# Optimization experiments

Hardware: AMD Instinct MI355X
Metric: run time of the kernel (lower is better)

The kernel has to match this reference:

```python
import jax, jax.numpy as jnp
import numpy as np

T_MAX = 0.5
LN_EPS = 1e-5
B, N, D = 256, 16384, 512
NNZ = N * 33  # ~ (2*top_k+1) nonzeros per row of the sparse Laplacian
DF = 4 * D
DT = 32  # time-embedding hidden size


def _layernorm(x, g, b):
    mu = jnp.mean(x, axis=-1, keepdims=True)
    var = jnp.mean((x - mu) ** 2, axis=-1, keepdims=True)
    return (x - mu) * jax.lax.rsqrt(var + LN_EPS) * g + b


def setup_inputs() -> dict:
    key = jax.random.key(0)
    ks = jax.random.split(key, 16)

    def lin_w(k, fan_out, fan_in):
        return jax.random.normal(k, (fan_out, fan_in), jnp.float32) * (1.0 / np.sqrt(fan_in))

    inp = {}
    inp["x0"] = jax.random.uniform(ks[0], (B, N), jnp.float32)
    inp["t"] = jax.random.uniform(ks[1], (B,), jnp.float32)
    inp["L_vals"] = jax.random.normal(ks[2], (NNZ,), jnp.float32) * 0.1
    inp["W_in"] = lin_w(ks[3], D, N)
    inp["b_in"] = jnp.zeros((D,), jnp.float32)
    inp["W_out"] = lin_w(ks[4], N, D)
    inp["b_out"] = jnp.zeros((N,), jnp.float32)
    inp["W_qkv"] = lin_w(ks[5], 3 * D, D)
    inp["b_qkv"] = jnp.zeros((3 * D,), jnp.float32)
    inp["W_o"] = lin_w(ks[6], D, D)
    inp["b_o"] = jnp.zeros((D,), jnp.float32)
    inp["g1"] = jnp.ones((D,), jnp.float32)
    inp["be1"] = jnp.zeros((D,), jnp.float32)
    inp["g2"] = jnp.ones((D,), jnp.float32)
    inp["be2"] = jnp.zeros((D,), jnp.float32)
    inp["W_f1"] = lin_w(ks[7], DF, D)
    inp["b_f1"] = jnp.zeros((DF,), jnp.float32)
    inp["W_f2"] = lin_w(ks[8], D, DF)
    inp["b_f2"] = jnp.zeros((D,), jnp.float32)
    inp["W_t1"] = lin_w(ks[9], DT, 1)
    inp["b_t1"] = jnp.zeros((DT,), jnp.float32)
    inp["W_t2"] = lin_w(ks[10], D, DT)
    inp["b_t2"] = jnp.zeros((D,), jnp.float32)
    inp["L_rows"] = jax.random.randint(ks[11], (NNZ,), 0, N, jnp.int32)
    inp["L_cols"] = jax.random.randint(ks[12], (NNZ,), 0, N, jnp.int32)
    return inp


def reference(x0, t, L_vals, W_in, b_in, W_out, b_out, W_qkv, b_qkv, W_o, b_o,
              g1, be1, g2, be2, W_f1, b_f1, W_f2, b_f2, W_t1, b_t1, W_t2, b_t2,
              L_rows, L_cols):
    n_items = x0.shape[1]
    d_model = W_in.shape[0]
    t_cont = t * T_MAX  # per-sample diffusion time (explicit input, not RNG)

    # Batched sparse Laplacian diffusion (replaces the per-row torch.sparse.mm loop):
    # (L @ x.T)[i, b] = sum_e L_vals[e] * x0[b, L_cols[e]] aggregated to row L_rows[e]
    contrib = x0[:, L_cols] * L_vals                                  # (B, NNZ)
    Lx = jax.ops.segment_sum(contrib.T, L_rows, num_segments=n_items)  # (N, B)
    x_t = x0 - t_cont[:, None] * Lx.T                                  # (B, N)

    # Denoiser (eval mode: dropout off)
    h = x_t @ W_in.T + b_in                                            # (B, D)
    t_norm = t_cont / T_MAX
    te = jax.nn.silu(t_norm[:, None] @ W_t1.T + b_t1) @ W_t2.T + b_t2  # (B, D)
    h = h + te

    # MultiheadAttention on a length-1 sequence: softmax over one key is exactly 1,
    # so attn_out = out_proj(V) with V = h @ W_v.T + b_v.
    qkv = h @ W_qkv.T + b_qkv                                          # (B, 3D)
    v = qkv[:, 2 * d_model:]
    attn_out = v @ W_o.T + b_o

    h = _layernorm(h + attn_out, g1, be1)
    ff = jax.nn.gelu(h @ W_f1.T + b_f1, approximate=False) @ W_f2.T + b_f2
    h = _layernorm(h + ff, g2, be2)

    pred = h @ W_out.T + b_out                                         # (B, N)
    return jnp.mean((pred - x0) ** 2)
```

## Files before the change

### kernel.cpp

```cpp
#include <hip/hip_runtime.h>
#include <math.h>

#define Bb   256
#define Nn   16384
#define Dd   512
#define NNZn 540672
#define DFf  2048
#define SLOT 64

#define CVT_BLKS 4736
#define TR_BLKS  1024
#define BK_BLKS  2112
#define PREP_BLKS (CVT_BLKS + TR_BLKS + BK_BLKS)

#define C1 65536
#define C2 131072
#define C3 393216
#define C4 655360
#define C5 2752512
#define C6 4849664

typedef __bf16 bf16;
typedef __bf16 bf16x4 __attribute__((ext_vector_type(4)));
typedef __bf16 bf16x8 __attribute__((ext_vector_type(8)));
typedef float  f32x4  __attribute__((ext_vector_type(4)));

__device__ __forceinline__ void gload16(const void* g, void* l) {
  __builtin_amdgcn_global_load_lds(
      (const __attribute__((address_space(1))) unsigned int*)g,
      (__attribute__((address_space(3))) unsigned int*)l, 16, 0, 0);
}

template <int NK>
__device__ __forceinline__ void bar_keep() {
  asm volatile("s_waitcnt vmcnt(%0) lgkmcnt(0)" :: "n"(NK) : "memory");
  __builtin_amdgcn_s_barrier();
}

__device__ __forceinline__ float f16_of(unsigned e) {
  unsigned short us = (unsigned short)(e & 0xffff);
  _Float16 h;
  __builtin_memcpy(&h, &us, 2);
  return (float)h;
}

__global__ __launch_bounds__(256) void k_prep(
    const float* __restrict__ w_v, const float* __restrict__ w_o,
    const float* __restrict__ w_f1, const float* __restrict__ w_f2,
    const float* __restrict__ w_in, const float* __restrict__ w_out,
    bf16* __restrict__ o_v, bf16* __restrict__ o_o,
    bf16* __restrict__ o_f1, bf16* __restrict__ o_f2,
    bf16* __restrict__ o_in, bf16* __restrict__ o_out,
    const float* __restrict__ x0, bf16* __restrict__ x0T,
    const int* __restrict__ rows, const int* __restrict__ cols,
    const float* __restrict__ vals,
    int* __restrict__ counts, unsigned* __restrict__ ents) {
  __shared__ float tile[64][65];
  int blk = blockIdx.x;
  int q = blk / 3;
  if ((blk % 3) == 0 && q < BK_BLKS) {
    int i = q * 256 + threadIdx.x;
    int r = rows[i];
    int p = atomicAdd(&counts[r], 1);
    if (p < SLOT) {
      _Float16 hv = (_Float16)vals[i];
      unsigned short us;
      __builtin_memcpy(&us, &hv, 2);
      ents[(size_t)r * SLOT + p] = ((unsigned)cols[i] << 16) | (unsigned)us;
    }
  } else {
    int sB = (blk + 2) / 3; if (sB > BK_BLKS) sB = BK_BLKS;
    int o = blk - sB;
    if (o < CVT_BLKS) {
      int v0i = o * 1024 + threadIdx.x;
#pragma unroll
      for (int j = 0; j < 4; j++) {
        int v = v0i + j * 256;
        const float* s; bf16* d; int base;
        if (v < C2)      { if (v < C1) { s = w_v;  d = o_v;  base = 0;  }
                           else        { s = w_o;  d = o_o;  base = C1; } }
        else if (v < C4) { if (v < C3) { s = w_f1; d = o_f1; base = C2; }
                           else        { s = w_f2; d = o_f2; base = C3; } }
        else             { if (v < C5) { s = w_in; d = o_in; base = C4; }
                           else        { s = w_out; d = o_out; base = C5; } }
        int idx = (v - base) * 4;
        float4 x = *(const float4*)(s + idx);
        bf16x4 ob;
        ob[0] = (bf16)x.x; ob[1] = (bf16)x.y; ob[2] = (bf16)x.z; ob[3] = (bf16)x.w;
        *(bf16x4*)(d + idx) = ob;
      }
    } else {
      int bx = o - CVT_BLKS;
      int n0 = (bx & 255) * 64, b0 = (bx >> 8) * 64;
      int tx = threadIdx.x & 63, ty = threadIdx.x >> 6;
#pragma unroll
      for (int i = 0; i < 16; i++) {
        int bl = ty * 16 + i;
        tile[bl][tx] = x0[(size_t)(b0 + bl) * Nn + n0 + tx];
      }
      __syncthreads();
#pragma unroll
      for (int i = 0; i < 16; i++) {
        int nl = ty * 16 + i;
        x0T[(size_t)(n0 + nl) * Bb + b0 + tx] = (bf16)tile[tx][nl];
      }
    }
  }
}

__global__ __launch_bounds__(256) void k_lx(const bf16x4* __restrict__ x0T4,
                                            const int* __restrict__ counts,
                                            const unsigned* __restrict__ ents,
                                            bf16x4* __restrict__ Lx4) {
  int w = threadIdx.x >> 6, lane = threadIdx.x & 63;
  int r = blockIdx.x * 4 + w;
  __shared__ unsigned esm[4][64];
  int cnt = counts[r];
  if (cnt > SLOT) cnt = SLOT;
  const unsigned* ep = ents + (size_t)r * SLOT;
  float a0 = 0.f, a1 = 0.f, a2 = 0.f, a3 = 0.f;
  float b0 = 0.f, b1 = 0.f, b2 = 0.f, b3 = 0.f;
  float c0 = 0.f, c1 = 0.f, c2 = 0.f, c3 = 0.f;
  float d0 = 0.f, d1 = 0.f, d2 = 0.f, d3 = 0.f;
  for (int base = 0; base < cnt; base += 64) {
    int m = cnt - base; if (m > 64) m = 64;
    if (lane < m) esm[w][lane] = ep[base + lane];
    int i = 0;
    for (; i + 3 < m; i += 4) {
      unsigned e0 = esm[w][i],     e1 = esm[w][i + 1];
      unsigned e2 = esm[w][i + 2], e3 = esm[w][i + 3];
      bf16x4 xv0 = x0T4[(size_t)(e0 >> 16) * 64 + lane];
      bf16x4 xv1 = x0T4[(size_t)(e1 >> 16) * 64 + lane];
      bf16x4 xv2 = x0T4[(size_t)(e2 >> 16) * 64 + lane];
      bf16x4 xv3 = x0T4[(size_t)(e3 >> 16) * 64 + lane];
      float v0 = f16_of(e0), v1 = f16_of(e1), v2 = f16_of(e2), v3 = f16_of(e3);
      a0 += v0 * (float)xv0[0]; a1 += v0 * (float)xv0[1];
      a2 += v0 * (float)xv0[2]; a3 += v0 * (float)xv0[3];
      b0 += v1 * (float)xv1[0]; b1 += v1 * (float)xv1[1];
      b2 += v1 * (float)xv1[2]; b3 += v1 * (float)xv1[3];
      c0 += v2 * (float)xv2[0]; c1 += v2 * (float)xv2[1];
      c2 += v2 * (float)xv2[2]; c3 += v2 * (float)xv2[3];
      d0 += v3 * (float)xv3[0]; d1 += v3 * (float)xv3[1];
      d2 += v3 * (float)xv3[2]; d3 += v3 * (float)xv3[3];
    }
    for (; i < m; i++) {
      unsigned e0 = esm[w][i];
      bf16x4 xv0 = x0T4[(size_t)(e0 >> 16) * 64 + lane];
      float v0 = f16_of(e0);
      a0 += v0 * (float)xv0[0]; a1 += v0 * (float)xv0[1];
      a2 += v0 * (float)xv0[2]; a3 += v0 * (float)xv0[3];
    }
  }
  bf16x4 o;
  o[0] = (bf16)(a0 + b0 + c0 + d0); o[1] = (bf16)(a1 + b1 + c1 + d1);
  o[2] = (bf16)(a2 + b2 + c2 + d2); o[3] = (bf16)(a3 + b3 + c3 + d3);
  Lx4[(size_t)r * 64 + lane] = o;
}

__global__ __launch_bounds__(256) void k_combine(const float* __restrict__ x0,
                                                 const bf16* __restrict__ Lx,
                                                 const float* __restrict__ t,
                                                 bf16* __restrict__ xt) {
  __shared__ float lxs[64][65];
  int n0 = blockIdx.x * 64, b0 = blockIdx.y * 64;
  int tx = threadIdx.x & 63, ty = threadIdx.x >> 6;
#pragma unroll
  for (int i = 0; i < 16; i++) {
    int nl = ty * 16 + i;
    lxs[nl][tx] = (float)Lx[(size_t)(n0 + nl) * Bb + b0 + tx];
  }
  __syncthreads();
#pragma unroll
  for (int i = 0; i < 16; i++) {
    int bl = ty * 16 + i;
    int b  = b0 + bl;
    float tc = t[b] * 0.5f;
    float v = x0[(size_t)b * Nn + n0 + tx] - tc * lxs[tx][bl];
    xt[(size_t)b * Nn + n0 + tx] = (bf16)v;
  }
}

template <int BM, int BN, int MODE, int ACT = 0>
__global__ __launch_bounds__(256) void gemm_tn(
    const bf16* __restrict__ A, const bf16* __restrict__ Bm,
    float* __restrict__ C, int N, int K, int kLen, int MN,
    const float* __restrict__ bias, const float* __restrict__ x0,
    float* __restrict__ lossOut) {
  constexpr int WM = BM / 2, WN = BN / 2, FM = WM / 16, FN = WN / 16;
  constexpr int PASS = (BM + BN) / 64;
  constexpr int KEEP = PASS;
  __shared__ __align__(16) bf16 As[3][BM * 32];
  __shared__ __align__(16) bf16 Bs[3][BN * 32];
  __shared__ float lred[4];
  const int tid = threadIdx.x;
  const int lane = tid & 63, w = tid >> 6;
  const int wm = w >> 1, wn = w & 1;
  const int mBase = blockIdx.x * BM, nBase = blockIdx.y * BN;
  const int k0 = blockIdx.z * kLen;
  const int nIter = kLen >> 5;

  f32x4 acc[FM][FN];
#pragma unroll
  for (int i = 0; i < FM; i++)
#pragma unroll
    for (int j = 0; j < FN; j++) acc[i][j] = {0.f, 0.f, 0.f, 0.f};

  auto stage = [&](int buf, int k) {
#pragma unroll
    for (int p = 0; p < PASS; p++) {
      int c = p * 4 + w;
      int u = c * 64 + lane;
      if (c < BM / 16) {
        int row = u >> 2, sub = u & 3;
        gload16(A + (size_t)(mBase + row) * K + k + sub * 8,
                (char*)As[buf] + c * 1024);
      } else {
        int u2 = u - BM * 4;
        int row = u2 >> 2, sub = u2 & 3;
        gload16(Bm + (size_t)(nBase + row) * K + k + sub * 8,
                (char*)Bs[buf] + (c - BM / 16) * 1024);
      }
    }
  };
  auto compute = [&](int cur) {
    bf16x8 af[FM], bfr[FN];
#pragma unroll
    for (int i = 0; i < FM; i++)
      af[i] = *(const bf16x8*)(As[cur] + (wm * WM + i * 16 + (lane & 15)) * 32 + (lane >> 4) * 8);
#pragma unroll
    for (int j = 0; j < FN; j++)
      bfr[j] = *(const bf16x8*)(Bs[cur] + (wn * WN + j * 16 + (lane & 15)) * 32 + (lane >> 4) * 8);
#pragma unroll
    for (int i = 0; i < FM; i++)
#pragma unroll
      for (int j = 0; j < FN; j++)
        acc[i][j] = __builtin_amdgcn_mfma_f32_16x16x32_bf16(af[i], bfr[j], acc[i][j], 0, 0, 0);
  };

  stage(0, k0);
  if (nIter > 1) {
    stage(1, k0 + 32);
    bar_keep<KEEP>();
  } else {
    bar_keep<0>();
  }

  int c0 = 0, c1 = 1, c2 = 2;
  for (int t = 0; t < nIter; t += 2) {
    {
      const bool more2 = (t + 2 < nIter);
      if (more2) stage(c2, k0 + (t + 2) * 32);
      compute(c0);
      if (more2) bar_keep<KEEP>(); else bar_keep<0>();
    }
    {
      const bool more2 = (t + 3 < nIter);
      if (more2) stage(c0, k0 + (t + 3) * 32);
      compute(c1);
      if (more2) bar_keep<KEEP>(); else bar_keep<0>();
    }
    int tmp = c2; c2 = c1; c1 = c0; c0 = tmp;
  }

  if constexpr (MODE == 0) {
    float* Cz = C + (size_t)blockIdx.z * MN;
#pragma unroll
    for (int i = 0; i < FM; i++)
#pragma unroll
      for (int j = 0; j < FN; j++) {
        int n  = nBase + wn * WN + j * 16 + (lane & 15);
        int mB = mBase + wm * WM + i * 16 + ((lane >> 4) << 2);
#pragma unroll
        for (int r = 0; r < 4; r++)
          Cz[(size_t)(mB + r) * N + n] = acc[i][j][r];
      }
  } else if constexpr (MODE == 1) {
    bf16* Cb = (bf16*)C;
#pragma unroll
    for (int i = 0; i < FM; i++)
#pragma unroll
      for (int j = 0; j < FN; j++) {
        int n  = nBase + wn * WN + j * 16 + (lane & 15);
        float bo = bias[n];
        int mB = mBase + wm * WM + i * 16 + ((lane >> 4) << 2);
#pragma unroll
        for (int r = 0; r < 4; r++) {
          float x = acc[i][j][r] + bo;
          if constexpr (ACT == 1)
            x = 0.5f * x * (1.f + erff(x * 0.70710678118654752f));
          Cb[(size_t)(mB + r) * N + n] = (bf16)x;
        }
      }
  } else {
    float lsum = 0.f;
#pragma unroll
    for (int i = 0; i < FM; i++)
#pragma unroll
      for (int j = 0; j < FN; j++) {
        int n  = nBase + wn * WN + j * 16 + (lane & 15);
        float bo = bias[n];
        int mB = mBase + wm * WM + i * 16 + ((lane >> 4) << 2);
#pragma unroll
        for (int r = 0; r < 4; r++) {
          float d = acc[i][j][r] + bo - x0[(size_t)(mB + r) * N + n];
          lsum += d * d;
        }
      }
    for (int off = 32; off > 0; off >>= 1) lsum += __shfl_down(lsum, off, 64);
    if (lane == 0) lred[w] = lsum;
    __syncthreads();
    if (tid == 0)
      atomicAdd(lossOut, lred[0] + lred[1] + lred[2] + lred[3]);
  }
}

__global__ __launch_bounds__(512) void k_epi_h(const float* __restrict__ P,
                                               const float* __restrict__ t,
                                               const float* __restrict__ W_t1,
                                               const float* __restrict__ b_t1,
                                               const float* __restrict__ W_t2,
                                               const float* __restrict__ b_t2,
                                               const float* __restrict__ b_in,
                                               float* __restrict__ h_f32,
                                               bf16* __restrict__ h_b) {
  int b = blockIdx.x, d = threadIdx.x;
  __shared__ float s[32];
  if (d < 32) {
    float z = t[b] * W_t1[d] + b_t1[d];
    s[d] = z / (1.f + expf(-z));
  }
  __syncthreads();
  int i = b * Dd + d;
  float v = b_in[d] + b_t2[d];
#pragma unroll
  for (int sp = 0; sp < 32; sp++) v += P[sp * (Bb * Dd) + i];
#pragma unroll
  for (int j = 0; j < 32; j++) v += s[j] * W_t2[d * 32 + j];
  h_f32[i] = v;
  h_b[i] = (bf16)v;
}

template <int NS>
__global__ __launch_bounds__(512) void k_ln(const float* __restrict__ base,
                                            const float* __restrict__ add,
                                            const float* __restrict__ bias,
                                            const float* __restrict__ g,
                                            const float* __restrict__ be,
                                            float* __restrict__ out_f32,
                                            bf16* __restrict__ out_b) {
  int b = blockIdx.x, d = threadIdx.x;
  __shared__ float red[16];
  int i = b * Dd + d;
  float x = base[i] + bias[d];
#pragma unroll
  for (int sp = 0; sp < NS; sp++) x += add[sp * (Bb * Dd) + i];
  int w = d >> 6, lane = d & 63;
  float s = x;
  for (int off = 32; off > 0; off >>= 1) s += __shfl_down(s, off, 64);
  if (lane == 0) red[w] = s;
  __syncthreads();
  if (d == 0) {
    float tot = 0.f;
    for (int q = 0; q < 8; q++) tot += red[q];
    red[8] = tot * (1.f / 512.f);
  }
  __syncthreads();
  float mu = red[8];
  float c = x - mu;
  float s2 = c * c;
  for (int off = 32; off > 0; off >>= 1) s2 += __shfl_down(s2, off, 64);
  if (lane == 0) red[w] = s2;
  __syncthreads();
  if (d == 0) {
    float tot = 0.f;
    for (int q = 0; q < 8; q++) tot += red[q];
    red[8] = tot * (1.f / 512.f);
  }
  __syncthreads();
  float var = red[8];
  float y = c * rsqrtf(var + 1e-5f) * g[d] + be[d];
  if (out_f32) out_f32[i] = y;
  out_b[i] = (bf16)y;
}

__global__ void k_final(const float* __restrict__ loss, float* __restrict__ out) {
  if (threadIdx.x == 0 && blockIdx.x == 0)
    out[0] = loss[0] * (1.f / 4194304.f);
}

extern "C" void kernel_launch(void* const* d_in, const int* in_sizes, int n_in,
                              void* d_out, int out_size, void* d_ws, size_t ws_size,
                              hipStream_t stream) {
  const float* x0    = (const float*)d_in[0];
  const float* t     = (const float*)d_in[1];
  const float* Lv    = (const float*)d_in[2];
  const float* W_in  = (const float*)d_in[3];
  const float* b_in  = (const float*)d_in[4];
  const float* W_out = (const float*)d_in[5];
  const float* b_out = (const float*)d_in[6];
  const float* W_qkv = (const float*)d_in[7];
  const float* b_qkv = (const float*)d_in[8];
  const float* W_o   = (const float*)d_in[9];
  const float* b_o   = (const float*)d_in[10];
  const float* g1    = (const float*)d_in[11];
  const float* be1   = (const float*)d_in[12];
  const float* g2    = (const float*)d_in[13];
  const float* be2   = (const float*)d_in[14];
  const float* W_f1  = (const float*)d_in[15];
  const float* b_f1  = (const float*)d_in[16];
  const float* W_f2  = (const float*)d_in[17];
  const float* b_f2  = (const float*)d_in[18];
  const float* W_t1  = (const float*)d_in[19];
  const float* b_t1  = (const float*)d_in[20];
  const float* W_t2  = (const float*)d_in[21];
  const float* b_t2  = (const float*)d_in[22];
  const int* L_rows  = (const int*)d_in[23];
  const int* L_cols  = (const int*)d_in[24];

  size_t off = 0;
  char* ws = (char*)d_ws;
  auto carve = [&](size_t bytes) -> void* {
    void* p = ws + off;
    off += (bytes + 255) & ~(size_t)255;
    return p;
  };

  bf16* W_v_b    = (bf16*)carve((size_t)Dd * Dd * 2);
  bf16* W_o_b    = (bf16*)carve((size_t)Dd * Dd * 2);
  bf16* W_f1_b   = (bf16*)carve((size_t)DFf * Dd * 2);
  bf16* W_f2_b   = (bf16*)carve((size_t)Dd * DFf * 2);
  bf16* W_in_b   = (bf16*)carve((size_t)Dd * Nn * 2);
  bf16* W_out_b  = (bf16*)carve((size_t)Nn * Dd * 2);
  bf16* x0T_b    = (bf16*)carve((size_t)Nn * Bb * 2);
  bf16* Lx_b     = (bf16*)carve((size_t)Nn * Bb * 2);
  bf16* xt_b     = (bf16*)carve((size_t)Bb * Nn * 2);
  float* p_h     = (float*)carve((size_t)32 * Bb * Dd * 4);
  float* p_at    = (float*)carve((size_t)Bb * Dd * 4);
  float* p_f2    = (float*)carve((size_t)4 * Bb * Dd * 4);
  float* h_f32   = (float*)carve((size_t)Bb * Dd * 4);
  bf16* h_b      = (bf16*)carve((size_t)Bb * Dd * 2);
  bf16* v_b      = (bf16*)carve((size_t)Bb * Dd * 2);
  float* hln_f32 = (float*)carve((size_t)Bb * Dd * 4);
  bf16* hln_b    = (bf16*)carve((size_t)Bb * Dd * 2);
  bf16* f1_b     = (bf16*)carve((size_t)Bb * DFf * 2);
  bf16* h2_b     = (bf16*)carve((size_t)Bb * Dd * 2);
  int* counts    = (int*)carve((size_t)Nn * 4);
  float* lossw   = (float*)carve(256);
  unsigned* ents = (unsigned*)carve((size_t)Nn * SLOT * 4);
  (void)in_sizes; (void)n_in; (void)out_size; (void)ws_size; (void)Lv;

  hipMemsetAsync(counts, 0, (size_t)Nn * 4 + 256, stream);

  k_prep<<<PREP_BLKS, 256, 0, stream>>>(
      W_qkv + (size_t)2 * Dd * Dd, W_o, W_f1, W_f2, W_in, W_out,
      W_v_b, W_o_b, W_f1_b, W_f2_b, W_in_b, W_out_b,
      x0, x0T_b, L_rows, L_cols, Lv, counts, ents);

  k_lx<<<Nn / 4, 256, 0, stream>>>((const bf16x4*)x0T_b, counts, ents,
                                   (bf16x4*)Lx_b);
  k_combine<<<dim3(256, 4), 256, 0, stream>>>(x0, Lx_b, t, xt_b);

  gemm_tn<128, 64, 0><<<dim3(2, 8, 32), 256, 0, stream>>>(
      xt_b, W_in_b, p_h, Dd, Nn, 512, Bb * Dd, nullptr, nullptr, nullptr);
  k_epi_h<<<Bb, 512, 0, stream>>>(p_h, t, W_t1, b_t1, W_t2, b_t2, b_in, h_f32, h_b);

  gemm_tn<32, 32, 1><<<dim3(8, 16, 1), 256, 0, stream>>>(
      h_b, W_v_b, (float*)v_b, Dd, Dd, 512, 0, b_qkv + 2 * Dd, nullptr, nullptr);

  gemm_tn<32, 32, 0><<<dim3(8, 16, 1), 256, 0, stream>>>(
      v_b, W_o_b, p_at, Dd, Dd, 512, 0, nullptr, nullptr, nullptr);
  k_ln<1><<<Bb, 512, 0, stream>>>(h_f32, p_at, b_o, g1, be1, hln_f32, hln_b);

  gemm_tn<32, 32, 1, 1><<<dim3(8, 64, 1), 256, 0, stream>>>(
      hln_b, W_f1_b, (float*)f1_b, DFf, Dd, 512, 0, b_f1, nullptr, nullptr);

  gemm_tn<32, 32, 0><<<dim3(8, 16, 4), 256, 0, stream>>>(
      f1_b, W_f2_b, p_f2, Dd, DFf, 512, Bb * Dd, nullptr, nullptr, nullptr);
  k_ln<4><<<Bb, 512, 0, stream>>>(hln_f32, p_f2, b_f2, g2, be2, nullptr, h2_b);

  gemm_tn<128, 64, 2><<<dim3(2, 256, 1), 256, 0, stream>>>(
      h2_b, W_out_b, nullptr, Nn, Dd, 512, 0, b_out, x0, lossw);
  k_final<<<1, 64, 0, stream>>>(lossw, (float*)d_out);
}
```

Before: 284.2 us.

## Move weight bf16 conversion from prep kernel into sparse gather kernel

The fp32-to-bf16 weight conversion moves out of the prep kernel and into the Laplacian gather kernel, with gather and conversion blocks interleaved. The prep kernel now only builds the x0 transpose and the sparse row buckets. The aim is to let bandwidth-heavy conversion traffic overlap the latency-bound random gathers rather than sharing a launch with the atomic-heavy bucketing. The conversion loads and stores are also made nontemporal to reduce cache pollution, at the cost of a bigger kernel with divergent block roles that may raise register pressure.

```diff
diff --git a/kernel.cpp b/kernel.cpp
--- a/kernel.cpp
+++ b/kernel.cpp
@@ -8,10 +8,12 @@
 #define DFf  2048
 #define SLOT 64
 
-#define CVT_BLKS 4736
 #define TR_BLKS  1024
 #define BK_BLKS  2112
-#define PREP_BLKS (CVT_BLKS + TR_BLKS + BK_BLKS)
+#define PREP0_BLKS (TR_BLKS + BK_BLKS)
+
+#define CVT_BLKS 4736
+#define LXP_BLKS (4096 + CVT_BLKS)
 
 #define C1 65536
 #define C2 131072
@@ -44,22 +46,31 @@
   return (float)h;
 }
 
-__global__ __launch_bounds__(256) void k_prep(
-    const float* __restrict__ w_v, const float* __restrict__ w_o,
-    const float* __restrict__ w_f1, const float* __restrict__ w_f2,
-    const float* __restrict__ w_in, const float* __restrict__ w_out,
-    bf16* __restrict__ o_v, bf16* __restrict__ o_o,
-    bf16* __restrict__ o_f1, bf16* __restrict__ o_f2,
-    bf16* __restrict__ o_in, bf16* __restrict__ o_out,
+__global__ __launch_bounds__(256) void k_prep0(
     const float* __restrict__ x0, bf16* __restrict__ x0T,
     const int* __restrict__ rows, const int* __restrict__ cols,
     const float* __restrict__ vals,
     int* __restrict__ counts, unsigned* __restrict__ ents) {
   __shared__ float tile[64][65];
   int blk = blockIdx.x;
-  int q = blk / 3;
-  if ((blk % 3) == 0 && q < BK_BLKS) {
-    int i = q * 256 + threadIdx.x;
+  if ((blk % 3) == 0 && blk / 3 < TR_BLKS) {
+    int bx = blk / 3;
+    int n0 = (bx & 255) * 64, b0 = (bx >> 8) * 64;
+    int tx = threadIdx.x & 63, ty = threadIdx.x >> 6;
+#pragma unroll
+    for (int i = 0; i < 16; i++) {
+      int bl = ty * 16 + i;
+      tile[bl][tx] = x0[(size_t)(b0 + bl) * Nn + n0 + tx];
+    }
+    __syncthreads();
+#pragma unroll
+    for (int i = 0; i < 16; i++) {
+      int nl = ty * 16 + i;
+      x0T[(size_t)(n0 + nl) * Bb + b0 + tx] = (bf16)tile[tx][nl];
+    }
+  } else {
+    int pre = (blk + 2) / 3; if (pre > TR_BLKS) pre = TR_BLKS;
+    int i = (blk - pre) * 256 + threadIdx.x;
     int r = rows[i];
     int p = atomicAdd(&counts[r], 1);
     if (p < SLOT) {
@@ -68,52 +79,50 @@
       __builtin_memcpy(&us, &hv, 2);
       ents[(size_t)r * SLOT + p] = ((unsigned)cols[i] << 16) | (unsigned)us;
     }
-  } else {
-    int sB = (blk + 2) / 3; if (sB > BK_BLKS) sB = BK_BLKS;
-    int o = blk - sB;
-    if (o < CVT_BLKS) {
-      int v0i = o * 1024 + threadIdx.x;
-#pragma unroll
-      for (int j = 0; j < 4; j++) {
-        int v = v0i + j * 256;
-        const float* s; bf16* d; int base;
-        if (v < C2)      { if (v < C1) { s = w_v;  d = o_v;  base = 0;  }
-                           else        { s = w_o;  d = o_o;  base = C1; } }
-        else if (v < C4) { if (v < C3) { s = w_f1; d = o_f1; base = C2; }
-                           else        { s = w_f2; d = o_f2; base = C3; } }
-        else             { if (v < C5) { s = w_in; d = o_in; base = C4; }
-                           else        { s = w_out; d = o_out; base = C5; } }
-        int idx = (v - base) * 4;
-        float4 x = *(const float4*)(s + idx);
-        bf16x4 ob;
-        ob[0] = (bf16)x.x; ob[1] = (bf16)x.y; ob[2] = (bf16)x.z; ob[3] = (bf16)x.w;
-        *(bf16x4*)(d + idx) = ob;
-      }
-    } else {
-      int bx = o - CVT_BLKS;
-      int n0 = (bx & 255) * 64, b0 = (bx >> 8) * 64;
-      int tx = threadIdx.x & 63, ty = threadIdx.x >> 6;
-#pragma unroll
-      for (int i = 0; i < 16; i++) {
-        int bl = ty * 16 + i;
-        tile[bl][tx] = x0[(size_t)(b0 + bl) * Nn + n0 + tx];
-      }
-      __syncthreads();
-#pragma unroll
-      for (int i = 0; i < 16; i++) {
-        int nl = ty * 16 + i;
-        x0T[(size_t)(n0 + nl) * Bb + b0 + tx] = (bf16)tile[tx][nl];
-      }
-    }
-  }
-}
-
-__global__ __launch_bounds__(256) void k_lx(const bf16x4* __restrict__ x0T4,
-                                            const int* __restrict__ counts,
-                                            const unsigned* __restrict__ ents,
-                                            bf16x4* __restrict__ Lx4) {
+  }
+}
+
+__global__ __launch_bounds__(256) void k_lxp(
+    const bf16x4* __restrict__ x0T4, const int* __restrict__ counts,
+    const unsigned* __restrict__ ents, bf16x4* __restrict__ Lx4,
+    const float* __restrict__ w_v, const float* __restrict__ w_o,
+    const float* __restrict__ w_f1, const float* __restrict__ w_f2,
+    const float* __restrict__ w_in, const float* __restrict__ w_out,
+    bf16* __restrict__ o_v, bf16* __restrict__ o_o,
+    bf16* __restrict__ o_f1, bf16* __restrict__ o_f2,
+    bf16* __restrict__ o_in, bf16* __restrict__ o_out) {
+  int blk = blockIdx.x;
+  bool isGather = (blk < 8192) && ((blk & 1) == 0);
+  if (!isGather) {
+    int co = (blk < 8192) ? (blk >> 1) : (blk - 4096);
+    const float* s; bf16* d; int base;
+    if (co < 128)      { if (co < 64)   { s = w_v;  d = o_v;  base = 0;  }
+                         else           { s = w_o;  d = o_o;  base = C1; } }
+    else if (co < 640) { if (co < 384)  { s = w_f1; d = o_f1; base = C2; }
+                         else           { s = w_f2; d = o_f2; base = C3; } }
+    else               { if (co < 2688) { s = w_in; d = o_in; base = C4; }
+                         else           { s = w_out; d = o_out; base = C5; } }
+    int rel = co * 1024 - base + threadIdx.x;
+    const f32x4* sv = (const f32x4*)s;
+    f32x4 x0v = __builtin_nontemporal_load(sv + rel);
+    f32x4 x1v = __builtin_nontemporal_load(sv + rel + 256);
+    f32x4 x2v = __builtin_nontemporal_load(sv + rel + 512);
+    f32x4 x3v = __builtin_nontemporal_load(sv + rel + 768);
+    bf16x4 o0, o1, o2, o3;
+    o0[0] = (bf16)x0v[0]; o0[1] = (bf16)x0v[1]; o0[2] = (bf16)x0v[2]; o0[3] = (bf16)x0v[3];
+    o1[0] = (bf16)x1v[0]; o1[1] = (bf16)x1v[1]; o1[2] = (bf16)x1v[2]; o1[3] = (bf16)x1v[3];
+    o2[0] = (bf16)x2v[0]; o2[1] = (bf16)x2v[1]; o2[2] = (bf16)x2v[2]; o2[3] = (bf16)x2v[3];
+    o3[0] = (bf16)x3v[0]; o3[1] = (bf16)x3v[1]; o3[2] = (bf16)x3v[2]; o3[3] = (bf16)x3v[3];
+    bf16x4* dv = (bf16x4*)d;
+    __builtin_nontemporal_store(o0, dv + rel);
+    __builtin_nontemporal_store(o1, dv + rel + 256);
+    __builtin_nontemporal_store(o2, dv + rel + 512);
+    __builtin_nontemporal_store(o3, dv + rel + 768);
+    return;
+  }
+  int gq = blk >> 1;
   int w = threadIdx.x >> 6, lane = threadIdx.x & 63;
-  int r = blockIdx.x * 4 + w;
+  int r = gq * 4 + w;
   __shared__ unsigned esm[4][64];
   int cnt = counts[r];
   if (cnt > SLOT) cnt = SLOT;
@@ -451,13 +460,14 @@
 
   hipMemsetAsync(counts, 0, (size_t)Nn * 4 + 256, stream);
 
-  k_prep<<<PREP_BLKS, 256, 0, stream>>>(
+  k_prep0<<<PREP0_BLKS, 256, 0, stream>>>(
+      x0, x0T_b, L_rows, L_cols, Lv, counts, ents);
+
+  k_lxp<<<LXP_BLKS, 256, 0, stream>>>(
+      (const bf16x4*)x0T_b, counts, ents, (bf16x4*)Lx_b,
       W_qkv + (size_t)2 * Dd * Dd, W_o, W_f1, W_f2, W_in, W_out,
-      W_v_b, W_o_b, W_f1_b, W_f2_b, W_in_b, W_out_b,
-      x0, x0T_b, L_rows, L_cols, Lv, counts, ents);
-
-  k_lx<<<Nn / 4, 256, 0, stream>>>((const bf16x4*)x0T_b, counts, ents,
-                                   (bf16x4*)Lx_b);
+      W_v_b, W_o_b, W_f1_b, W_f2_b, W_in_b, W_out_b);
+
   k_combine<<<dim3(256, 4), 256, 0, stream>>>(x0, Lx_b, t, xt_b);
 
   gemm_tn<128, 64, 0><<<dim3(2, 8, 32), 256, 0, stream>>>(
```

Result: slower. 310.4 us (+9.2%).

## Fuse fp32-to-bf16 conversion of W_in/W_out into GEMM B-tile loads

Applied to the files above, without the earlier changes.

Stops pre-converting the two large weight matrices W_in and W_out to bf16 in the prep kernel. The two large GEMMs now load fp32 B tiles into registers, convert them, and write bf16 into LDS inside the pipelined loop. This removes a full write and re-read of about 32 MB of bf16 weights. In exchange the GEMM reads twice as many bytes for B and adds register staging and conversion work to its inner loop. The prep kernel's block interleaving is also generalised, and its small-weight conversion now uses nontemporal loads and stores.

```diff
diff --git a/kernel.cpp b/kernel.cpp
--- a/kernel.cpp
+++ b/kernel.cpp
@@ -8,17 +8,10 @@
 #define DFf  2048
 #define SLOT 64
 
-#define CVT_BLKS 4736
+#define CVT_BLKS 640
 #define TR_BLKS  1024
 #define BK_BLKS  2112
-#define PREP_BLKS (CVT_BLKS + TR_BLKS + BK_BLKS)
-
-#define C1 65536
-#define C2 131072
-#define C3 393216
-#define C4 655360
-#define C5 2752512
-#define C6 4849664
+#define PREP_TOT (CVT_BLKS + TR_BLKS + BK_BLKS)
 
 typedef __bf16 bf16;
 typedef __bf16 bf16x4 __attribute__((ext_vector_type(4)));
@@ -47,19 +40,18 @@
 __global__ __launch_bounds__(256) void k_prep(
     const float* __restrict__ w_v, const float* __restrict__ w_o,
     const float* __restrict__ w_f1, const float* __restrict__ w_f2,
-    const float* __restrict__ w_in, const float* __restrict__ w_out,
     bf16* __restrict__ o_v, bf16* __restrict__ o_o,
     bf16* __restrict__ o_f1, bf16* __restrict__ o_f2,
-    bf16* __restrict__ o_in, bf16* __restrict__ o_out,
     const float* __restrict__ x0, bf16* __restrict__ x0T,
     const int* __restrict__ rows, const int* __restrict__ cols,
     const float* __restrict__ vals,
     int* __restrict__ counts, unsigned* __restrict__ ents) {
   __shared__ float tile[64][65];
   int blk = blockIdx.x;
-  int q = blk / 3;
-  if ((blk % 3) == 0 && q < BK_BLKS) {
-    int i = q * 256 + threadIdx.x;
+  int before = (int)(((long long)blk * BK_BLKS) / PREP_TOT);
+  bool isB = (int)(((long long)(blk + 1) * BK_BLKS) / PREP_TOT) > before;
+  if (isB) {
+    int i = before * 256 + threadIdx.x;
     int r = rows[i];
     int p = atomicAdd(&counts[r], 1);
     if (p < SLOT) {
@@ -69,26 +61,29 @@
       ents[(size_t)r * SLOT + p] = ((unsigned)cols[i] << 16) | (unsigned)us;
     }
   } else {
-    int sB = (blk + 2) / 3; if (sB > BK_BLKS) sB = BK_BLKS;
-    int o = blk - sB;
+    int o = blk - before;
     if (o < CVT_BLKS) {
-      int v0i = o * 1024 + threadIdx.x;
-#pragma unroll
-      for (int j = 0; j < 4; j++) {
-        int v = v0i + j * 256;
-        const float* s; bf16* d; int base;
-        if (v < C2)      { if (v < C1) { s = w_v;  d = o_v;  base = 0;  }
-                           else        { s = w_o;  d = o_o;  base = C1; } }
-        else if (v < C4) { if (v < C3) { s = w_f1; d = o_f1; base = C2; }
-                           else        { s = w_f2; d = o_f2; base = C3; } }
-        else             { if (v < C5) { s = w_in; d = o_in; base = C4; }
-                           else        { s = w_out; d = o_out; base = C5; } }
-        int idx = (v - base) * 4;
-        float4 x = *(const float4*)(s + idx);
-        bf16x4 ob;
-        ob[0] = (bf16)x.x; ob[1] = (bf16)x.y; ob[2] = (bf16)x.z; ob[3] = (bf16)x.w;
-        *(bf16x4*)(d + idx) = ob;
-      }
+      const float* s; bf16* d; int base;
+      if (o < 128) { if (o < 64)  { s = w_v;  d = o_v;  base = 0;      }
+                     else         { s = w_o;  d = o_o;  base = 65536;  } }
+      else         { if (o < 384) { s = w_f1; d = o_f1; base = 131072; }
+                     else         { s = w_f2; d = o_f2; base = 393216; } }
+      int rel = o * 1024 - base + threadIdx.x;
+      const f32x4* sv = (const f32x4*)s;
+      f32x4 x0v = __builtin_nontemporal_load(sv + rel);
+      f32x4 x1v = __builtin_nontemporal_load(sv + rel + 256);
+      f32x4 x2v = __builtin_nontemporal_load(sv + rel + 512);
+      f32x4 x3v = __builtin_nontemporal_load(sv + rel + 768);
+      bf16x4 o0, o1, o2, o3;
+      o0[0] = (bf16)x0v[0]; o0[1] = (bf16)x0v[1]; o0[2] = (bf16)x0v[2]; o0[3] = (bf16)x0v[3];
+      o1[0] = (bf16)x1v[0]; o1[1] = (bf16)x1v[1]; o1[2] = (bf16)x1v[2]; o1[3] = (bf16)x1v[3];
+      o2[0] = (bf16)x2v[0]; o2[1] = (bf16)x2v[1]; o2[2] = (bf16)x2v[2]; o2[3] = (bf16)x2v[3];
+      o3[0] = (bf16)x3v[0]; o3[1] = (bf16)x3v[1]; o3[2] = (bf16)x3v[2]; o3[3] = (bf16)x3v[3];
+      bf16x4* dv = (bf16x4*)d;
+      __builtin_nontemporal_store(o0, dv + rel);
+      __builtin_nontemporal_store(o1, dv + rel + 256);
+      __builtin_nontemporal_store(o2, dv + rel + 512);
+      __builtin_nontemporal_store(o3, dv + rel + 768);
     } else {
       int bx = o - CVT_BLKS;
       int n0 = (bx & 255) * 64, b0 = (bx >> 8) * 64;
@@ -180,15 +175,16 @@
   }
 }
 
-template <int BM, int BN, int MODE, int ACT = 0>
+template <int BM, int BN, int MODE, int ACT = 0, int BF32 = 0>
 __global__ __launch_bounds__(256) void gemm_tn(
-    const bf16* __restrict__ A, const bf16* __restrict__ Bm,
+    const bf16* __restrict__ A, const void* __restrict__ Bmv,
     float* __restrict__ C, int N, int K, int kLen, int MN,
     const float* __restrict__ bias, const float* __restrict__ x0,
     float* __restrict__ lossOut) {
   constexpr int WM = BM / 2, WN = BN / 2, FM = WM / 16, FN = WN / 16;
   constexpr int PASS = (BM + BN) / 64;
-  constexpr int KEEP = PASS;
+  constexpr int PA   = (BM * 64) / 4096;
+  constexpr int NB   = BN / 32;
   __shared__ __align__(16) bf16 As[3][BM * 32];
   __shared__ __align__(16) bf16 Bs[3][BN * 32];
   __shared__ float lred[4];
@@ -205,23 +201,6 @@
 #pragma unroll
     for (int j = 0; j < FN; j++) acc[i][j] = {0.f, 0.f, 0.f, 0.f};
 
-  auto stage = [&](int buf, int k) {
-#pragma unroll
-    for (int p = 0; p < PASS; p++) {
-      int c = p * 4 + w;
-      int u = c * 64 + lane;
-      if (c < BM / 16) {
-        int row = u >> 2, sub = u & 3;
-        gload16(A + (size_t)(mBase + row) * K + k + sub * 8,
-                (char*)As[buf] + c * 1024);
-      } else {
-        int u2 = u - BM * 4;
-        int row = u2 >> 2, sub = u2 & 3;
-        gload16(Bm + (size_t)(nBase + row) * K + k + sub * 8,
-                (char*)Bs[buf] + (c - BM / 16) * 1024);
-      }
-    }
-  };
   auto compute = [&](int cur) {
     bf16x8 af[FM], bfr[FN];
 #pragma unroll
@@ -237,29 +216,103 @@
         acc[i][j] = __builtin_amdgcn_mfma_f32_16x16x32_bf16(af[i], bfr[j], acc[i][j], 0, 0, 0);
   };
 
-  stage(0, k0);
-  if (nIter > 1) {
-    stage(1, k0 + 32);
-    bar_keep<KEEP>();
+  if constexpr (!BF32) {
+    const bf16* Bm = (const bf16*)Bmv;
+    auto stage = [&](int buf, int k) {
+#pragma unroll
+      for (int p = 0; p < PASS; p++) {
+        int c = p * 4 + w;
+        int u = c * 64 + lane;
+        if (c < BM / 16) {
+          int row = u >> 2, sub = u & 3;
+          gload16(A + (size_t)(mBase + row) * K + k + sub * 8,
+                  (char*)As[buf] + c * 1024);
+        } else {
+          int u2 = u - BM * 4;
+          int row = u2 >> 2, sub = u2 & 3;
+          gload16(Bm + (size_t)(nBase + row) * K + k + sub * 8,
+                  (char*)Bs[buf] + (c - BM / 16) * 1024);
+        }
+      }
+    };
+    stage(0, k0);
+    if (nIter > 1) { stage(1, k0 + 32); bar_keep<PASS>(); }
+    else bar_keep<0>();
+    int c0 = 0, c1 = 1, c2 = 2;
+    for (int t = 0; t < nIter; t += 2) {
+      {
+        const bool more2 = (t + 2 < nIter);
+        if (more2) stage(c2, k0 + (t + 2) * 32);
+        compute(c0);
+        if (more2) bar_keep<PASS>(); else bar_keep<0>();
+      }
+      {
+        const bool more3 = (t + 3 < nIter);
+        if (more3) stage(c0, k0 + (t + 3) * 32);
+        compute(c1);
+        if (more3) bar_keep<PASS>(); else bar_keep<0>();
+      }
+      int tmp = c2; c2 = c1; c1 = c0; c0 = tmp;
+    }
   } else {
-    bar_keep<0>();
-  }
-
-  int c0 = 0, c1 = 1, c2 = 2;
-  for (int t = 0; t < nIter; t += 2) {
-    {
-      const bool more2 = (t + 2 < nIter);
-      if (more2) stage(c2, k0 + (t + 2) * 32);
-      compute(c0);
-      if (more2) bar_keep<KEEP>(); else bar_keep<0>();
-    }
-    {
-      const bool more2 = (t + 3 < nIter);
-      if (more2) stage(c0, k0 + (t + 3) * 32);
-      compute(c1);
-      if (more2) bar_keep<KEEP>(); else bar_keep<0>();
-    }
-    int tmp = c2; c2 = c1; c1 = c0; c0 = tmp;
+    const float* Bf = (const float*)Bmv;
+    float4 bA[NB], bB[NB];
+    auto stageA = [&](int buf, int k) {
+#pragma unroll
+      for (int p = 0; p < PA; p++) {
+        int u = p * 256 + tid;
+        gload16(A + (size_t)(mBase + (u >> 2)) * K + k + (u & 3) * 8,
+                (char*)As[buf] + p * 4096 + w * 1024);
+      }
+    };
+    auto loadBreg = [&](float4* br, int k) {
+#pragma unroll
+      for (int p = 0; p < NB; p++) {
+        int u = p * 256 + tid;
+        int row = u >> 3, sub = u & 7;
+        br[p] = *(const float4*)(Bf + (size_t)(nBase + row) * K + k + sub * 4);
+      }
+    };
+    auto storeBreg = [&](const float4* br, int buf) {
+#pragma unroll
+      for (int p = 0; p < NB; p++) {
+        int u = p * 256 + tid;
+        int row = u >> 3, sub = u & 7;
+        bf16x4 o;
+        o[0] = (bf16)br[p].x; o[1] = (bf16)br[p].y;
+        o[2] = (bf16)br[p].z; o[3] = (bf16)br[p].w;
+        *(bf16x4*)(Bs[buf] + row * 32 + sub * 4) = o;
+      }
+    };
+    loadBreg(bA, k0);
+    storeBreg(bA, 0);
+    stageA(0, k0);
+    if (nIter > 1) {
+      stageA(1, k0 + 32);
+      loadBreg(bB, k0 + 32);
+      bar_keep<PA + NB>();
+    } else {
+      bar_keep<0>();
+    }
+    int c0 = 0, c1 = 1, c2 = 2;
+    for (int t = 0; t < nIter; t += 2) {
+      {
+        const bool more2 = (t + 2 < nIter);
+        if (more2) { stageA(c2, k0 + (t + 2) * 32); loadBreg(bA, k0 + (t + 2) * 32); }
+        compute(c0);
+        storeBreg(bB, c1);
+        if (more2) bar_keep<PA + NB>(); else bar_keep<0>();
+      }
+      {
+        const bool more2 = (t + 2 < nIter);
+        const bool more3 = (t + 3 < nIter);
+        if (more3) { stageA(c0, k0 + (t + 3) * 32); loadBreg(bB, k0 + (t + 3) * 32); }
+        compute(c1);
+        if (more2) storeBreg(bA, c2);
+        if (more3) bar_keep<PA + NB>(); else bar_keep<0>();
+      }
+      int tmp = c2; c2 = c1; c1 = c0; c0 = tmp;
+    }
   }
 
   if constexpr (MODE == 0) {
@@ -429,8 +482,6 @@
   bf16* W_o_b    = (bf16*)carve((size_t)Dd * Dd * 2);
   bf16* W_f1_b   = (bf16*)carve((size_t)DFf * Dd * 2);
   bf16* W_f2_b   = (bf16*)carve((size_t)Dd * DFf * 2);
-  bf16* W_in_b   = (bf16*)carve((size_t)Dd * Nn * 2);
-  bf16* W_out_b  = (bf16*)carve((size_t)Nn * Dd * 2);
   bf16* x0T_b    = (bf16*)carve((size_t)Nn * Bb * 2);
   bf16* Lx_b     = (bf16*)carve((size_t)Nn * Bb * 2);
   bf16* xt_b     = (bf16*)carve((size_t)Bb * Nn * 2);
@@ -451,17 +502,17 @@
 
   hipMemsetAsync(counts, 0, (size_t)Nn * 4 + 256, stream);
 
-  k_prep<<<PREP_BLKS, 256, 0, stream>>>(
-      W_qkv + (size_t)2 * Dd * Dd, W_o, W_f1, W_f2, W_in, W_out,
-      W_v_b, W_o_b, W_f1_b, W_f2_b, W_in_b, W_out_b,
+  k_prep<<<PREP_TOT, 256, 0, stream>>>(
+      W_qkv + (size_t)2 * Dd * Dd, W_o, W_f1, W_f2,
+      W_v_b, W_o_b, W_f1_b, W_f2_b,
       x0, x0T_b, L_rows, L_cols, Lv, counts, ents);
 
   k_lx<<<Nn / 4, 256, 0, stream>>>((const bf16x4*)x0T_b, counts, ents,
                                    (bf16x4*)Lx_b);
   k_combine<<<dim3(256, 4), 256, 0, stream>>>(x0, Lx_b, t, xt_b);
 
-  gemm_tn<128, 64, 0><<<dim3(2, 8, 32), 256, 0, stream>>>(
-      xt_b, W_in_b, p_h, Dd, Nn, 512, Bb * Dd, nullptr, nullptr, nullptr);
+  gemm_tn<128, 64, 0, 0, 1><<<dim3(2, 8, 32), 256, 0, stream>>>(
+      xt_b, W_in, p_h, Dd, Nn, 512, Bb * Dd, nullptr, nullptr, nullptr);
   k_epi_h<<<Bb, 512, 0, stream>>>(p_h, t, W_t1, b_t1, W_t2, b_t2, b_in, h_f32, h_b);
 
   gemm_tn<32, 32, 1><<<dim3(8, 16, 1), 256, 0, stream>>>(
@@ -478,7 +529,7 @@
       f1_b, W_f2_b, p_f2, Dd, DFf, 512, Bb * Dd, nullptr, nullptr, nullptr);
   k_ln<4><<<Bb, 512, 0, stream>>>(hln_f32, p_f2, b_f2, g2, be2, nullptr, h2_b);
 
-  gemm_tn<128, 64, 2><<<dim3(2, 256, 1), 256, 0, stream>>>(
-      h2_b, W_out_b, nullptr, Nn, Dd, 512, 0, b_out, x0, lossw);
+  gemm_tn<128, 64, 2, 0, 1><<<dim3(2, 256, 1), 256, 0, stream>>>(
+      h2_b, W_out, nullptr, Nn, Dd, 512, 0, b_out, x0, lossw);
   k_final<<<1, 64, 0, stream>>>(lossw, (float*)d_out);
 }
```

New measurement: 298.6 us. +5.1%, slower.
